# Kernel optimization log

Measured on AMD Instinct MI355X. Metric: run time of the kernel, lower is better.

Reference implementation:

```python
import jax, jax.numpy as jnp
import numpy as np

T, H = 2048, 1024          # tokens, hidden_size
NH, NKV, D = 16, 4, 64     # heads, kv heads, head_dim
E, F = 8, 1024             # experts, intermediate_size
TOPK = 1
EPS = 1e-5
THETA = 500000.0
SCALE = D ** -0.5


def rmsnorm(x, w=None, eps=EPS):
    # fp32 accumulation like vLLM RMSNorm
    v = jnp.mean(x.astype(jnp.float32) ** 2, axis=-1, keepdims=True)
    y = x.astype(jnp.float32) * jax.lax.rsqrt(v + eps)
    y = y.astype(x.dtype)
    return y * w if w is not None else y


def setup_inputs() -> dict:
    key = jax.random.key(0)
    ks = jax.random.split(key, 12)
    s = 1.0 / np.sqrt(H)
    sf = 1.0 / np.sqrt(F)
    return {
        "positions": jnp.arange(T, dtype=jnp.int32),
        "hidden_states": jax.random.normal(ks[0], (T, H), jnp.float32),
        "ln1_w": jnp.ones((H,), jnp.float32),
        "ln2_w": jnp.ones((H,), jnp.float32),
        "wqkv": jax.random.normal(ks[1], (H, (NH + 2 * NKV) * D), jnp.float32) * s,
        "wo": jax.random.normal(ks[2], (NH * D, H), jnp.float32) * s,
        "router_w": jax.random.normal(ks[3], (H, E), jnp.float32) * s,
        "w_gate": jax.random.normal(ks[4], (E, H, F), jnp.float32) * s,
        "w_up": jax.random.normal(ks[5], (E, H, F), jnp.float32) * s,
        "w_down": jax.random.normal(ks[6], (E, F, H), jnp.float32) * sf,
        "sh_gate": jax.random.normal(ks[7], (H, F), jnp.float32) * s,
        "sh_up": jax.random.normal(ks[8], (H, F), jnp.float32) * s,
        "sh_down": jax.random.normal(ks[9], (F, H), jnp.float32) * sf,
    }


def reference(positions, hidden_states, ln1_w, ln2_w, wqkv, wo, router_w,
              w_gate, w_up, w_down, sh_gate, sh_up, sh_down):
    # --- input_layernorm (residual is None on first call) ---
    residual = hidden_states
    h = rmsnorm(hidden_states, ln1_w)

    # --- attention: qkv proj ---
    qkv = h @ wqkv
    q = qkv[:, : NH * D].reshape(T, NH, D)
    k = qkv[:, NH * D: (NH + NKV) * D].reshape(T, NKV, D)
    v = qkv[:, (NH + NKV) * D:].reshape(T, NKV, D)

    # --- neox-style RoPE ---
    half = D // 2
    inv_freq = 1.0 / (THETA ** (jnp.arange(half, dtype=jnp.float32) / half))
    ang = positions.astype(jnp.float32)[:, None] * inv_freq[None, :]
    cos = jnp.cos(ang)[:, None, :]  # [T,1,half]
    sin = jnp.sin(ang)[:, None, :]

    def rope(x):
        x1, x2 = x[..., :half], x[..., half:]
        return jnp.concatenate([x1 * cos - x2 * sin, x2 * cos + x1 * sin], axis=-1)

    q = rope(q)
    k = rope(k)

    # --- fp32 QK-RMSNorm (no weight), applied after RoPE as in source ---
    q = rmsnorm(q)
    k = rmsnorm(k)

    # --- GQA causal attention ---
    n_rep = NH // NKV
    kr = jnp.repeat(k, n_rep, axis=1)  # [T,NH,D]
    vr = jnp.repeat(v, n_rep, axis=1)
    scores = jnp.einsum('thd,shd->hts', q, kr) * SCALE  # [NH,T,T]
    causal = positions[:, None] >= positions[None, :]
    scores = jnp.where(causal[None], scores, -jnp.inf)
    attn = jax.nn.softmax(scores, axis=-1)
    ao = jnp.einsum('hts,shd->thd', attn, vr).reshape(T, NH * D)
    h = ao @ wo

    # --- post_attention_layernorm with fused residual add ---
    x = h + residual
    residual = x
    h = rmsnorm(x, ln2_w)

    # --- MoE: top-1 sigmoid router, router weight applied on input ---
    logits = h @ router_w                      # [T,E]
    score, idx = jax.lax.top_k(logits, TOPK)   # [T,1]
    gate = jax.nn.sigmoid(score.astype(jnp.float32)).astype(h.dtype)
    x_in = h * gate                            # apply_router_weight_on_input
    onehot = (idx == jnp.arange(E)[None, :]).astype(h.dtype)  # [T,E]
    g = jax.nn.silu(jnp.einsum('th,ehf->tef', x_in, w_gate)) \
        * jnp.einsum('th,ehf->tef', x_in, w_up)               # [T,E,F]
    out_e = jnp.einsum('tef,efh->teh', g, w_down)             # [T,E,H]
    routed = jnp.einsum('teh,te->th', out_e, onehot)

    # --- shared expert (SiLU MLP) ---
    shared = (jax.nn.silu(h @ sh_gate) * (h @ sh_up)) @ sh_down

    out = routed + shared
    return (out, residual)
```

## Files before the change

kernel.cpp:

```cpp
#include <hip/hip_runtime.h>
#include <hip/hip_bf16.h>
#include <cmath>
#include <cstdint>

#define T 2048
#define H 1024
#define NH 16
#define NKV 4
#define DH 64
#define NE 8
#define FF 1024
#define QKVN ((NH + 2 * NKV) * DH)
#define EPS 1e-5f
#define ATTN_SCALE 0.125f
#define LOG2E 1.44269504f
#define MBOUND 12.0f

typedef short bf16x8 __attribute__((ext_vector_type(8)));
typedef float floatx4 __attribute__((ext_vector_type(4)));

__device__ __forceinline__ void gload16(const void* g, void* l) {
  __builtin_amdgcn_global_load_lds((const __attribute__((address_space(1))) void*)g,
                                   (__attribute__((address_space(3))) void*)l, 16, 0, 0);
}

__global__ __launch_bounds__(256) void rmsnorm1024(const float* __restrict__ x,
                                                   const float* __restrict__ w,
                                                   __hip_bfloat16* __restrict__ yb) {
  int row = blockIdx.x;
  const float4* x4 = (const float4*)(x + (size_t)row * H);
  float4 v = x4[threadIdx.x];
  float s = v.x * v.x + v.y * v.y + v.z * v.z + v.w * v.w;
  #pragma unroll
  for (int o = 32; o; o >>= 1) s += __shfl_down(s, o, 64);
  __shared__ float red[4];
  if ((threadIdx.x & 63) == 0) red[threadIdx.x >> 6] = s;
  __syncthreads();
  s = red[0] + red[1] + red[2] + red[3];
  float inv = rsqrtf(s * (1.0f / (float)H) + EPS);
  float4 wv = ((const float4*)w)[threadIdx.x];
  __hip_bfloat16* yp = yb + (size_t)row * H + threadIdx.x * 4;
  yp[0] = __float2bfloat16(v.x * inv * wv.x);
  yp[1] = __float2bfloat16(v.y * inv * wv.y);
  yp[2] = __float2bfloat16(v.z * inv * wv.z);
  yp[3] = __float2bfloat16(v.w * inv * wv.w);
}

__global__ __launch_bounds__(256) void fused_add_rms(const float* __restrict__ a,
                                                     const float* __restrict__ b,
                                                     float* __restrict__ resid,
                                                     const float* __restrict__ w,
                                                     float* __restrict__ yf,
                                                     __hip_bfloat16* __restrict__ yb) {
  int row = blockIdx.x;
  float4 av = ((const float4*)(a + (size_t)row * H))[threadIdx.x];
  float4 bv = ((const float4*)(b + (size_t)row * H))[threadIdx.x];
  float4 v = make_float4(av.x + bv.x, av.y + bv.y, av.z + bv.z, av.w + bv.w);
  ((float4*)(resid + (size_t)row * H))[threadIdx.x] = v;
  float s = v.x * v.x + v.y * v.y + v.z * v.z + v.w * v.w;
  #pragma unroll
  for (int o = 32; o; o >>= 1) s += __shfl_down(s, o, 64);
  __shared__ float red[4];
  if ((threadIdx.x & 63) == 0) red[threadIdx.x >> 6] = s;
  __syncthreads();
  s = red[0] + red[1] + red[2] + red[3];
  float inv = rsqrtf(s * (1.0f / (float)H) + EPS);
  float4 wv = ((const float4*)w)[threadIdx.x];
  float o0 = v.x * inv * wv.x, o1 = v.y * inv * wv.y, o2 = v.z * inv * wv.z, o3 = v.w * inv * wv.w;
  ((float4*)(yf + (size_t)row * H))[threadIdx.x] = make_float4(o0, o1, o2, o3);
  __hip_bfloat16* yp = yb + (size_t)row * H + threadIdx.x * 4;
  yp[0] = __float2bfloat16(o0);
  yp[1] = __float2bfloat16(o1);
  yp[2] = __float2bfloat16(o2);
  yp[3] = __float2bfloat16(o3);
}

__global__ __launch_bounds__(256) void tcast9(const float* __restrict__ srcE,
                                              const float* __restrict__ srcS,
                                              __hip_bfloat16* __restrict__ dst, int R, int C,
                                              long long srcStride, long long dstStride,
                                              long long sBatch, long long dBatch) {
  int z = blockIdx.z;
  const float* src = (srcS && z == (int)gridDim.z - 1) ? srcS : srcE + (long long)z * sBatch;
  dst += (long long)z * dBatch;
  int c0 = blockIdx.x * 64, r0 = blockIdx.y * 32;
  __shared__ float tile[32][65];
  int tid = threadIdx.x;
  int lr = tid >> 4;
  int lc = (tid & 15) * 4;
  #pragma unroll
  for (int it = 0; it < 2; it++) {
    float4 v = *(const float4*)(src + (long long)(r0 + lr + it * 16) * srcStride + c0 + lc);
    tile[lr + it * 16][lc + 0] = v.x;
    tile[lr + it * 16][lc + 1] = v.y;
    tile[lr + it * 16][lc + 2] = v.z;
    tile[lr + it * 16][lc + 3] = v.w;
  }
  __syncthreads();
  int oc = tid >> 2;
  int rr = (tid & 3) * 8;
  short ov[8];
  #pragma unroll
  for (int i = 0; i < 8; i++) {
    __hip_bfloat16 b = __float2bfloat16(tile[rr + i][oc]);
    ov[i] = *(short*)&b;
  }
  *(bf16x8*)((short*)dst + (long long)(c0 + oc) * dstStride + r0 + rr) = *(bf16x8*)ov;
}

__global__ __launch_bounds__(256) void gemm_bf16(const __hip_bfloat16* __restrict__ A,
                                                 const __hip_bfloat16* __restrict__ A2,
                                                 const __hip_bfloat16* __restrict__ Bt,
                                                 void* __restrict__ Cout, void* __restrict__ Cout2,
                                                 int M, int N, int K, int out_bf16,
                                                 const int* __restrict__ row_offs,
                                                 long long strideB) {
  int e = blockIdx.z;
  bool sh = (A2 != nullptr && e == (int)gridDim.z - 1);
  int rbeg = 0, rend = M;
  const __hip_bfloat16* Ap = A;
  void* Cp = Cout;
  if (sh) {
    Ap = A2; Cp = Cout2;
  } else if (row_offs) {
    rbeg = row_offs[e]; rend = row_offs[e + 1];
  }
  long long m0 = rbeg + (long long)blockIdx.y * 128;
  if (m0 >= rend) return;
  long long n0 = (long long)blockIdx.x * 64;
  const __hip_bfloat16* Bp = Bt + (long long)e * strideB;

  __shared__ unsigned short As[128 * 64];
  __shared__ unsigned short Bs[64 * 64];

  int tid = threadIdx.x;
  int lane = tid & 63, w = tid >> 6;
  int wr = (w >> 1) * 64, wc = (w & 1) * 32;
  int qd = lane >> 4, ln16 = lane & 15;
  int l7 = ln16 & 7;

  floatx4 acc[4][2];
  floatx4 zero = {0.f, 0.f, 0.f, 0.f};
  #pragma unroll
  for (int i = 0; i < 4; i++)
    #pragma unroll
    for (int j = 0; j < 2; j++) acc[i][j] = zero;

  int rowA[4], kcA[4];
  #pragma unroll
  for (int it = 0; it < 4; it++) {
    int chunk = tid + it * 256;
    rowA[it] = chunk >> 3;
    kcA[it] = ((chunk & 7) ^ (rowA[it] & 7)) * 8;
  }

  for (int k0 = 0; k0 < K; k0 += 64) {
    #pragma unroll
    for (int it = 0; it < 4; it++) {
      long long ra = m0 + rowA[it];
      if (ra >= rend) ra = rend - 1;
      gload16(Ap + ra * K + k0 + kcA[it], As + (tid + it * 256) * 8);
    }
    #pragma unroll
    for (int it = 0; it < 2; it++)
      gload16(Bp + (n0 + rowA[it]) * K + k0 + kcA[it], Bs + (tid + it * 256) * 8);
    __syncthreads();
    #pragma unroll
    for (int s = 0; s < 2; s++) {
      bf16x8 af[4], bfr[2];
      #pragma unroll
      for (int i = 0; i < 4; i++) {
        int row = wr + i * 16 + ln16;
        af[i] = *(const bf16x8*)(As + row * 64 + (((s * 4 + qd) ^ l7) * 8));
      }
      #pragma unroll
      for (int j = 0; j < 2; j++) {
        int row = wc + j * 16 + ln16;
        bfr[j] = *(const bf16x8*)(Bs + row * 64 + (((s * 4 + qd) ^ l7) * 8));
      }
      #pragma unroll
      for (int i = 0; i < 4; i++)
        #pragma unroll
        for (int j = 0; j < 2; j++)
          acc[i][j] = __builtin_amdgcn_mfma_f32_16x16x32_bf16(af[i], bfr[j], acc[i][j], 0, 0, 0);
    }
    __syncthreads();
  }

  #pragma unroll
  for (int i = 0; i < 4; i++) {
    #pragma unroll
    for (int r = 0; r < 4; r++) {
      long long gm = m0 + wr + i * 16 + qd * 4 + r;
      if (gm < rend) {
        #pragma unroll
        for (int j = 0; j < 2; j++) {
          long long gn = n0 + wc + j * 16 + ln16;
          float v = acc[i][j][r];
          if (out_bf16)
            ((__hip_bfloat16*)Cp)[gm * N + gn] = __float2bfloat16(v);
          else
            ((float*)Cp)[gm * N + gn] = v;
        }
      }
    }
  }
}

__global__ __launch_bounds__(256) void rope_pack(const float* __restrict__ qkv,
                                                 const int* __restrict__ positions,
                                                 __hip_bfloat16* __restrict__ Qb,
                                                 __hip_bfloat16* __restrict__ Kb) {
  int b = blockIdx.x * 4 + (threadIdx.x >> 6);
  int t = b / (NH + NKV);
  int hh = b % (NH + NKV);
  const float* ptr = qkv + (long long)t * QKVN + hh * DH;
  int d = threadIdx.x & 63;
  float v = ptr[d];
  int fi = d & 31;
  float inv_freq = exp2f(-(float)fi * (18.93156857f / 32.0f));
  float ang = (float)positions[t] * inv_freq;
  float c = __cosf(ang), s = __sinf(ang);
  float other = __shfl_xor(v, 32, 64);
  float r = (d < 32) ? (v * c - other * s) : (v * c + other * s);
  float sq = r * r;
  #pragma unroll
  for (int off = 32; off; off >>= 1) sq += __shfl_xor(sq, off, 64);
  float o = r * rsqrtf(sq * (1.0f / (float)DH) + EPS);
  if (hh < NH)
    Qb[(size_t)t * (NH * DH) + hh * DH + d] = __float2bfloat16(o * (ATTN_SCALE * LOG2E));
  else
    Kb[(size_t)t * (NKV * DH) + (hh - NH) * DH + d] = __float2bfloat16(o);
}

__global__ __launch_bounds__(256) void attn_mfma(const __hip_bfloat16* __restrict__ Qb,
                                                 const __hip_bfloat16* __restrict__ Kb,
                                                 const __hip_bfloat16* __restrict__ VtG,
                                                 __hip_bfloat16* __restrict__ ao) {
  int h = blockIdx.y;
  int kvh = h >> 2;
  int nb = gridDim.x;
  int bx = blockIdx.x;
  int qi = (bx & 1) ? (nb - 1 - (bx >> 1)) : (bx >> 1);
  int q0 = qi * 64;

  __shared__ unsigned short Ks[64 * 64];
  __shared__ unsigned short Vs[64 * 64];
  __shared__ unsigned short Ps[4 * 16 * 64];

  int tid = threadIdx.x;
  int lane = tid & 63, w = tid >> 6;
  int qd = lane >> 4, ln16 = lane & 15;
  int l7 = ln16 & 7;
  unsigned short* Pw = Ps + w * 16 * 64;

  int r0 = tid >> 3;
  int sc = ((tid & 7) ^ (r0 & 7)) * 8;

  int tq = q0 + w * 16 + ln16;
  const unsigned short* qp = (const unsigned short*)Qb + (size_t)tq * (NH * DH) + h * DH;
  bf16x8 aq[2];
  aq[0] = *(const bf16x8*)(qp + qd * 8);
  aq[1] = *(const bf16x8*)(qp + 32 + qd * 8);

  bf16x8 ones;
  #pragma unroll
  for (int i = 0; i < 8; i++) ones[i] = (short)0x3F80;

  floatx4 O_[4], accl;
  floatx4 zero = {0.f, 0.f, 0.f, 0.f};
  #pragma unroll
  for (int j = 0; j < 4; j++) O_[j] = zero;
  accl = zero;
  int tq_base = q0 + w * 16 + qd * 4;
  int wave_min_row = q0 + w * 16;

  for (int kb = 0; kb < q0 + 64; kb += 64) {
    gload16((const unsigned short*)Kb + (size_t)(kb + r0) * (NKV * DH) + kvh * DH + sc, Ks + tid * 8);
    gload16((const unsigned short*)Kb + (size_t)(kb + r0 + 32) * (NKV * DH) + kvh * DH + sc, Ks + tid * 8 + 2048);
    gload16((const unsigned short*)VtG + (size_t)(kvh * DH + r0) * T + kb + sc, Vs + tid * 8);
    gload16((const unsigned short*)VtG + (size_t)(kvh * DH + r0 + 32) * T + kb + sc, Vs + tid * 8 + 2048);
    __syncthreads();

    floatx4 S_[4];
    #pragma unroll
    for (int j = 0; j < 4; j++) S_[j] = zero;
    #pragma unroll
    for (int s = 0; s < 2; s++) {
      bf16x8 bk[4];
      #pragma unroll
      for (int j = 0; j < 4; j++)
        bk[j] = *(const bf16x8*)(Ks + (j * 16 + ln16) * 64 + (((s * 4 + qd) ^ l7) * 8));
      #pragma unroll
      for (int j = 0; j < 4; j++)
        S_[j] = __builtin_amdgcn_mfma_f32_16x16x32_bf16(aq[s], bk[j], S_[j], 0, 0, 0);
    }

    if (kb + 63 > wave_min_row) {
      #pragma unroll
      for (int j = 0; j < 4; j++) {
        int tk = kb + j * 16 + ln16;
        #pragma unroll
        for (int r = 0; r < 4; r++)
          S_[j][r] = (tk <= tq_base + r) ? exp2f(S_[j][r] - MBOUND) : 0.f;
      }
    } else {
      #pragma unroll
      for (int j = 0; j < 4; j++)
        #pragma unroll
        for (int r = 0; r < 4; r++) S_[j][r] = exp2f(S_[j][r] - MBOUND);
    }

    #pragma unroll
    for (int j = 0; j < 4; j++)
      #pragma unroll
      for (int r = 0; r < 4; r++) {
        int row = qd * 4 + r;
        int pc = (((j * 2 + (ln16 >> 3)) ^ (row & 7)) * 8) + l7;
        __hip_bfloat16 pb = __float2bfloat16(S_[j][r]);
        Pw[row * 64 + pc] = *(unsigned short*)&pb;
      }

    #pragma unroll
    for (int s = 0; s < 2; s++) {
      bf16x8 ap = *(const bf16x8*)(Pw + ln16 * 64 + (((s * 4 + qd) ^ l7) * 8));
      bf16x8 bv[4];
      #pragma unroll
      for (int j = 0; j < 4; j++)
        bv[j] = *(const bf16x8*)(Vs + (j * 16 + ln16) * 64 + (((s * 4 + qd) ^ l7) * 8));
      #pragma unroll
      for (int j = 0; j < 4; j++)
        O_[j] = __builtin_amdgcn_mfma_f32_16x16x32_bf16(ap, bv[j], O_[j], 0, 0, 0);
      accl = __builtin_amdgcn_mfma_f32_16x16x32_bf16(ap, ones, accl, 0, 0, 0);
    }
    __syncthreads();
  }

  float inv[4];
  #pragma unroll
  for (int r = 0; r < 4; r++) inv[r] = 1.0f / accl[r];
  #pragma unroll
  for (int j = 0; j < 4; j++)
    #pragma unroll
    for (int r = 0; r < 4; r++)
      ao[(size_t)(tq_base + r) * (NH * DH) + h * DH + j * 16 + ln16] =
          __float2bfloat16(O_[j][r] * inv[r]);
}

__global__ void silumul_both(const __hip_bfloat16* __restrict__ gA2,
                             const __hip_bfloat16* __restrict__ gS2,
                             __hip_bfloat16* __restrict__ gP,
                             __hip_bfloat16* __restrict__ gPs, int n4each) {
  int i = blockIdx.x * blockDim.x + threadIdx.x;
  const __hip_bfloat16* src = gA2;
  __hip_bfloat16* dst = gP;
  if (i >= n4each) {
    i -= n4each;
    src = gS2;
    dst = gPs;
  }
  int el = i * 4;
  int row = el >> 10;
  int c = el & (FF - 1);
  const __hip_bfloat16* g = src + (size_t)row * (2 * FF) + c;
  #pragma unroll
  for (int k = 0; k < 4; k++) {
    float av = __bfloat162float(g[k]);
    float bv = __bfloat162float(g[FF + k]);
    dst[el + k] = __float2bfloat16(av / (1.f + __expf(-av)) * bv);
  }
}

__global__ __launch_bounds__(64) void router_kernel(const float* __restrict__ h2,
                                                    const float* __restrict__ rw,
                                                    int* __restrict__ idx,
                                                    float* __restrict__ gate,
                                                    int* __restrict__ counts) {
  int t = blockIdx.x;
  int lane = threadIdx.x;
  float acc[NE] = {};
  for (int k = lane; k < H; k += 64) {
    float hv = h2[(long long)t * H + k];
    float4 r0 = *(const float4*)(rw + (long long)k * NE);
    float4 r1 = *(const float4*)(rw + (long long)k * NE + 4);
    acc[0] += hv * r0.x; acc[1] += hv * r0.y; acc[2] += hv * r0.z; acc[3] += hv * r0.w;
    acc[4] += hv * r1.x; acc[5] += hv * r1.y; acc[6] += hv * r1.z; acc[7] += hv * r1.w;
  }
  #pragma unroll
  for (int off = 32; off; off >>= 1)
    #pragma unroll
    for (int e2 = 0; e2 < NE; e2++) acc[e2] += __shfl_down(acc[e2], off, 64);
  if (lane == 0) {
    int best = 0;
    float bv = acc[0];
    #pragma unroll
    for (int e2 = 1; e2 < NE; e2++)
      if (acc[e2] > bv) { bv = acc[e2]; best = e2; }
    idx[t] = best;
    gate[t] = 1.f / (1.f + expf(-bv));
    atomicAdd(&counts[best], 1);
  }
}

__global__ void zero_counts_kernel(int* c) {
  if (threadIdx.x < 2 * NE) c[threadIdx.x] = 0;
}

__global__ void scan_kernel(const int* __restrict__ counts, int* __restrict__ offs) {
  if (threadIdx.x == 0) {
    int s = 0;
    for (int e2 = 0; e2 < NE; e2++) { offs[e2] = s; s += counts[e2]; }
    offs[NE] = s;
  }
}

__global__ void assign_kernel(const int* __restrict__ idx, const int* __restrict__ offs,
                              int* __restrict__ cnt2, int* __restrict__ perm,
                              int* __restrict__ pos) {
  int t = blockIdx.x * blockDim.x + threadIdx.x;
  if (t >= T) return;
  int e2 = idx[t];
  int p = offs[e2] + atomicAdd(&cnt2[e2], 1);
  pos[t] = p;
  perm[p] = t;
}

__global__ __launch_bounds__(256) void gather_kernel(const float* __restrict__ h2,
                                                     const float* __restrict__ gate,
                                                     const int* __restrict__ perm,
                                                     __hip_bfloat16* __restrict__ xg) {
  int p = blockIdx.x;
  int t = perm[p];
  float g = gate[t];
  float4 v = ((const float4*)(h2 + (long long)t * H))[threadIdx.x];
  __hip_bfloat16* yp = xg + (long long)p * H + threadIdx.x * 4;
  yp[0] = __float2bfloat16(v.x * g);
  yp[1] = __float2bfloat16(v.y * g);
  yp[2] = __float2bfloat16(v.z * g);
  yp[3] = __float2bfloat16(v.w * g);
}

__global__ __launch_bounds__(256) void final_add_kernel(float* __restrict__ out,
                                                        const float* __restrict__ outp,
                                                        const int* __restrict__ pos) {
  int t = blockIdx.x;
  int p = pos[t];
  const float4* src = (const float4*)(outp + (long long)p * H);
  float4* dst = (float4*)(out + (long long)t * H);
  float4 a = dst[threadIdx.x];
  float4 b = src[threadIdx.x];
  a.x += b.x; a.y += b.y; a.z += b.z; a.w += b.w;
  dst[threadIdx.x] = a;
}

extern "C" void kernel_launch(void* const* d_in, const int* in_sizes, int n_in,
                              void* d_out, int out_size, void* d_ws, size_t ws_size,
                              hipStream_t stream) {
  const int* positions = (const int*)d_in[0];
  const float* hidden = (const float*)d_in[1];
  const float* ln1_w = (const float*)d_in[2];
  const float* ln2_w = (const float*)d_in[3];
  const float* wqkv = (const float*)d_in[4];
  const float* wo = (const float*)d_in[5];
  const float* router_w = (const float*)d_in[6];
  const float* w_gate = (const float*)d_in[7];
  const float* w_up = (const float*)d_in[8];
  const float* w_down = (const float*)d_in[9];
  const float* sh_gate = (const float*)d_in[10];
  const float* sh_up = (const float*)d_in[11];
  const float* sh_down = (const float*)d_in[12];

  float* out = (float*)d_out;
  float* resid = out + (size_t)T * H;

  char* p = (char*)d_ws;
  auto alloc = [&](size_t bytes) { char* r = p; p += (bytes + 255) & ~(size_t)255; return r; };

  float* qkv = (float*)alloc((size_t)T * QKVN * 4);
  float* h2 = (float*)alloc((size_t)T * H * 4);
  float* gb1 = (float*)alloc((size_t)T * H * 4);
  float* outp = (float*)alloc((size_t)T * H * 4);
  __hip_bfloat16* h1b = (__hip_bfloat16*)alloc((size_t)T * H * 2);
  __hip_bfloat16* aob = (__hip_bfloat16*)alloc((size_t)T * H * 2);
  __hip_bfloat16* h2b = (__hip_bfloat16*)alloc((size_t)T * H * 2);
  __hip_bfloat16* xgb = (__hip_bfloat16*)alloc((size_t)T * H * 2);
  __hip_bfloat16* gA2 = (__hip_bfloat16*)alloc((size_t)T * 2 * FF * 2);
  __hip_bfloat16* gP = (__hip_bfloat16*)alloc((size_t)T * FF * 2);
  __hip_bfloat16* Qb = (__hip_bfloat16*)alloc((size_t)T * NH * DH * 2);
  __hip_bfloat16* Kb = (__hip_bfloat16*)alloc((size_t)T * NKV * DH * 2);
  __hip_bfloat16* VtG = (__hip_bfloat16*)alloc((size_t)NKV * DH * T * 2);
  __hip_bfloat16* wqkvT = (__hip_bfloat16*)alloc((size_t)H * QKVN * 2);
  __hip_bfloat16* woT = (__hip_bfloat16*)alloc((size_t)H * H * 2);
  __hip_bfloat16* wguT = (__hip_bfloat16*)alloc((size_t)9 * 2 * FF * H * 2);
  __hip_bfloat16* wdT = (__hip_bfloat16*)alloc((size_t)9 * H * FF * 2);
  int* counts = (int*)alloc(2 * NE * 4);
  int* cnt2 = counts + NE;
  int* offs = (int*)alloc((NE + 1) * 4);
  int* idx = (int*)alloc(T * 4);
  int* perm = (int*)alloc(T * 4);
  int* pos = (int*)alloc(T * 4);
  float* gate = (float*)alloc(T * 4);

  __hip_bfloat16* gS2 = (__hip_bfloat16*)gb1;
  __hip_bfloat16* gPs = h1b;

  tcast9<<<dim3(QKVN / 64, H / 32, 1), 256, 0, stream>>>(wqkv, nullptr, wqkvT, H, QKVN, QKVN, H, 0, 0);
  tcast9<<<dim3(H / 64, H / 32, 1), 256, 0, stream>>>(wo, nullptr, woT, H, H, H, H, 0, 0);
  tcast9<<<dim3(FF / 64, H / 32, 9), 256, 0, stream>>>(w_gate, sh_gate, wguT, H, FF, FF, H,
                                                       (long long)H * FF, (long long)2 * H * FF);
  tcast9<<<dim3(FF / 64, H / 32, 9), 256, 0, stream>>>(w_up, sh_up, wguT + (size_t)FF * H, H, FF, FF, H,
                                                       (long long)H * FF, (long long)2 * H * FF);
  tcast9<<<dim3(H / 64, FF / 32, 9), 256, 0, stream>>>(w_down, sh_down, wdT, FF, H, H, FF,
                                                       (long long)FF * H, (long long)H * FF);

  rmsnorm1024<<<T, 256, 0, stream>>>(hidden, ln1_w, h1b);
  gemm_bf16<<<dim3(QKVN / 64, T / 128, 1), 256, 0, stream>>>(h1b, nullptr, wqkvT, qkv, nullptr,
                                                             T, QKVN, H, 0, nullptr, 0);
  rope_pack<<<T * (NH + NKV) / 4, 256, 0, stream>>>(qkv, positions, Qb, Kb);
  tcast9<<<dim3(NKV * DH / 64, T / 32, 1), 256, 0, stream>>>(qkv + (NH + NKV) * DH, nullptr, VtG,
                                                             T, NKV * DH, QKVN, T, 0, 0);
  attn_mfma<<<dim3(T / 64, NH), 256, 0, stream>>>(Qb, Kb, VtG, aob);
  gemm_bf16<<<dim3(H / 64, T / 128, 1), 256, 0, stream>>>(aob, nullptr, woT, gb1, nullptr,
                                                          T, H, H, 0, nullptr, 0);
  fused_add_rms<<<T, 256, 0, stream>>>(gb1, hidden, resid, ln2_w, h2, h2b);
  zero_counts_kernel<<<1, 64, 0, stream>>>(counts);
  router_kernel<<<T, 64, 0, stream>>>(h2, router_w, idx, gate, counts);
  scan_kernel<<<1, 64, 0, stream>>>(counts, offs);
  assign_kernel<<<T / 256, 256, 0, stream>>>(idx, offs, cnt2, perm, pos);
  gather_kernel<<<T, 256, 0, stream>>>(h2, gate, perm, xgb);
  gemm_bf16<<<dim3(2 * FF / 64, T / 128, 9), 256, 0, stream>>>(xgb, h2b, wguT, gA2, gS2,
                                                               T, 2 * FF, H, 1, offs,
                                                               (long long)2 * H * FF);
  silumul_both<<<(2 * T * FF / 4) / 256, 256, 0, stream>>>(gA2, gS2, gP, gPs, T * FF / 4);
  gemm_bf16<<<dim3(H / 64, T / 128, 9), 256, 0, stream>>>(gP, gPs, wdT, outp, out,
                                                          T, H, FF, 0, offs, (long long)FF * H);
  final_add_kernel<<<T, 256, 0, stream>>>(out, outp, pos);
}
```

Before: 410.3 us.

## Double-buffer GEMM and attention LDS tiles, scatter MoE down-proj via atomics

Adds two-stage LDS double buffering to the bf16 GEMM and the attention kernel, so the next K/V or A/B tile is prefetched while MFMAs run on the current one. The down-projection GEMM now atomically adds its output straight into the zeroed output at the permuted token row. This removes the separate outp buffer and the final_add kernel. The assign and gather kernels are merged into one launch. The cost is doubled shared memory, which may lower occupancy, plus fp32 atomic traffic and a memset of the output.

```diff
diff --git a/kernel.cpp b/kernel.cpp
--- a/kernel.cpp
+++ b/kernel.cpp
@@ -112,9 +112,10 @@
                                                  const __hip_bfloat16* __restrict__ A2,
                                                  const __hip_bfloat16* __restrict__ Bt,
                                                  void* __restrict__ Cout, void* __restrict__ Cout2,
-                                                 int M, int N, int K, int out_bf16,
+                                                 int M, int N, int K, int out_mode,
                                                  const int* __restrict__ row_offs,
-                                                 long long strideB) {
+                                                 long long strideB,
+                                                 const int* __restrict__ permmap) {
   int e = blockIdx.z;
   bool sh = (A2 != nullptr && e == (int)gridDim.z - 1);
   int rbeg = 0, rend = M;
@@ -130,8 +131,8 @@
   long long n0 = (long long)blockIdx.x * 64;
   const __hip_bfloat16* Bp = Bt + (long long)e * strideB;
 
-  __shared__ unsigned short As[128 * 64];
-  __shared__ unsigned short Bs[64 * 64];
+  __shared__ unsigned short As[2 * 128 * 64];
+  __shared__ unsigned short Bs[2 * 64 * 64];
 
   int tid = threadIdx.x;
   int lane = tid & 63, w = tid >> 6;
@@ -147,36 +148,51 @@
     for (int j = 0; j < 2; j++) acc[i][j] = zero;
 
   int rowA[4], kcA[4];
+  long long raClamp[4];
   #pragma unroll
   for (int it = 0; it < 4; it++) {
     int chunk = tid + it * 256;
     rowA[it] = chunk >> 3;
     kcA[it] = ((chunk & 7) ^ (rowA[it] & 7)) * 8;
-  }
-
-  for (int k0 = 0; k0 < K; k0 += 64) {
-    #pragma unroll
-    for (int it = 0; it < 4; it++) {
-      long long ra = m0 + rowA[it];
-      if (ra >= rend) ra = rend - 1;
-      gload16(Ap + ra * K + k0 + kcA[it], As + (tid + it * 256) * 8);
-    }
-    #pragma unroll
-    for (int it = 0; it < 2; it++)
-      gload16(Bp + (n0 + rowA[it]) * K + k0 + kcA[it], Bs + (tid + it * 256) * 8);
-    __syncthreads();
+    long long ra = m0 + rowA[it];
+    raClamp[it] = (ra >= rend) ? (rend - 1) : ra;
+  }
+
+  int niter = K >> 6;
+  #pragma unroll
+  for (int it = 0; it < 4; it++)
+    gload16(Ap + raClamp[it] * K + kcA[it], As + (tid + it * 256) * 8);
+  #pragma unroll
+  for (int it = 0; it < 2; it++)
+    gload16(Bp + (n0 + rowA[it]) * K + kcA[it], Bs + (tid + it * 256) * 8);
+  __syncthreads();
+
+  for (int k = 0; k < niter; k++) {
+    int cur = k & 1;
+    if (k + 1 < niter) {
+      int nxt = cur ^ 1;
+      int k0 = (k + 1) << 6;
+      #pragma unroll
+      for (int it = 0; it < 4; it++)
+        gload16(Ap + raClamp[it] * K + k0 + kcA[it], As + nxt * 8192 + (tid + it * 256) * 8);
+      #pragma unroll
+      for (int it = 0; it < 2; it++)
+        gload16(Bp + (n0 + rowA[it]) * K + k0 + kcA[it], Bs + nxt * 4096 + (tid + it * 256) * 8);
+    }
+    const unsigned short* Asc = As + cur * 8192;
+    const unsigned short* Bsc = Bs + cur * 4096;
     #pragma unroll
     for (int s = 0; s < 2; s++) {
       bf16x8 af[4], bfr[2];
       #pragma unroll
       for (int i = 0; i < 4; i++) {
         int row = wr + i * 16 + ln16;
-        af[i] = *(const bf16x8*)(As + row * 64 + (((s * 4 + qd) ^ l7) * 8));
+        af[i] = *(const bf16x8*)(Asc + row * 64 + (((s * 4 + qd) ^ l7) * 8));
       }
       #pragma unroll
       for (int j = 0; j < 2; j++) {
         int row = wc + j * 16 + ln16;
-        bfr[j] = *(const bf16x8*)(Bs + row * 64 + (((s * 4 + qd) ^ l7) * 8));
+        bfr[j] = *(const bf16x8*)(Bsc + row * 64 + (((s * 4 + qd) ^ l7) * 8));
       }
       #pragma unroll
       for (int i = 0; i < 4; i++)
@@ -193,12 +209,15 @@
     for (int r = 0; r < 4; r++) {
       long long gm = m0 + wr + i * 16 + qd * 4 + r;
       if (gm < rend) {
+        long long gmo = (out_mode == 2 && !sh && permmap) ? permmap[gm] : gm;
         #pragma unroll
         for (int j = 0; j < 2; j++) {
           long long gn = n0 + wc + j * 16 + ln16;
           float v = acc[i][j][r];
-          if (out_bf16)
+          if (out_mode == 1)
             ((__hip_bfloat16*)Cp)[gm * N + gn] = __float2bfloat16(v);
+          else if (out_mode == 2)
+            atomicAdd(&((float*)Cp)[gmo * N + gn], v);
           else
             ((float*)Cp)[gm * N + gn] = v;
         }
@@ -244,8 +263,8 @@
   int qi = (bx & 1) ? (nb - 1 - (bx >> 1)) : (bx >> 1);
   int q0 = qi * 64;
 
-  __shared__ unsigned short Ks[64 * 64];
-  __shared__ unsigned short Vs[64 * 64];
+  __shared__ unsigned short Ks[2 * 64 * 64];
+  __shared__ unsigned short Vs[2 * 64 * 64];
   __shared__ unsigned short Ps[4 * 16 * 64];
 
   int tid = threadIdx.x;
@@ -275,12 +294,27 @@
   int tq_base = q0 + w * 16 + qd * 4;
   int wave_min_row = q0 + w * 16;
 
+  const unsigned short* KbU = (const unsigned short*)Kb;
+  const unsigned short* VtU = (const unsigned short*)VtG;
+
+  gload16(KbU + (size_t)(r0) * (NKV * DH) + kvh * DH + sc, Ks + tid * 8);
+  gload16(KbU + (size_t)(r0 + 32) * (NKV * DH) + kvh * DH + sc, Ks + tid * 8 + 2048);
+  gload16(VtU + (size_t)(kvh * DH + r0) * T + sc, Vs + tid * 8);
+  gload16(VtU + (size_t)(kvh * DH + r0 + 32) * T + sc, Vs + tid * 8 + 2048);
+  __syncthreads();
+
   for (int kb = 0; kb < q0 + 64; kb += 64) {
-    gload16((const unsigned short*)Kb + (size_t)(kb + r0) * (NKV * DH) + kvh * DH + sc, Ks + tid * 8);
-    gload16((const unsigned short*)Kb + (size_t)(kb + r0 + 32) * (NKV * DH) + kvh * DH + sc, Ks + tid * 8 + 2048);
-    gload16((const unsigned short*)VtG + (size_t)(kvh * DH + r0) * T + kb + sc, Vs + tid * 8);
-    gload16((const unsigned short*)VtG + (size_t)(kvh * DH + r0 + 32) * T + kb + sc, Vs + tid * 8 + 2048);
-    __syncthreads();
+    int cur = (kb >> 6) & 1;
+    if (kb < q0) {
+      int nxt = cur ^ 1;
+      int kn = kb + 64;
+      gload16(KbU + (size_t)(kn + r0) * (NKV * DH) + kvh * DH + sc, Ks + nxt * 4096 + tid * 8);
+      gload16(KbU + (size_t)(kn + r0 + 32) * (NKV * DH) + kvh * DH + sc, Ks + nxt * 4096 + tid * 8 + 2048);
+      gload16(VtU + (size_t)(kvh * DH + r0) * T + kn + sc, Vs + nxt * 4096 + tid * 8);
+      gload16(VtU + (size_t)(kvh * DH + r0 + 32) * T + kn + sc, Vs + nxt * 4096 + tid * 8 + 2048);
+    }
+    const unsigned short* Ksc = Ks + cur * 4096;
+    const unsigned short* Vsc = Vs + cur * 4096;
 
     floatx4 S_[4];
     #pragma unroll
@@ -290,7 +324,7 @@
       bf16x8 bk[4];
       #pragma unroll
       for (int j = 0; j < 4; j++)
-        bk[j] = *(const bf16x8*)(Ks + (j * 16 + ln16) * 64 + (((s * 4 + qd) ^ l7) * 8));
+        bk[j] = *(const bf16x8*)(Ksc + (j * 16 + ln16) * 64 + (((s * 4 + qd) ^ l7) * 8));
       #pragma unroll
       for (int j = 0; j < 4; j++)
         S_[j] = __builtin_amdgcn_mfma_f32_16x16x32_bf16(aq[s], bk[j], S_[j], 0, 0, 0);
@@ -327,7 +361,7 @@
       bf16x8 bv[4];
       #pragma unroll
       for (int j = 0; j < 4; j++)
-        bv[j] = *(const bf16x8*)(Vs + (j * 16 + ln16) * 64 + (((s * 4 + qd) ^ l7) * 8));
+        bv[j] = *(const bf16x8*)(Vsc + (j * 16 + ln16) * 64 + (((s * 4 + qd) ^ l7) * 8));
       #pragma unroll
       for (int j = 0; j < 4; j++)
         O_[j] = __builtin_amdgcn_mfma_f32_16x16x32_bf16(ap, bv[j], O_[j], 0, 0, 0);
@@ -414,23 +448,23 @@
   }
 }
 
-__global__ void assign_kernel(const int* __restrict__ idx, const int* __restrict__ offs,
-                              int* __restrict__ cnt2, int* __restrict__ perm,
-                              int* __restrict__ pos) {
-  int t = blockIdx.x * blockDim.x + threadIdx.x;
-  if (t >= T) return;
-  int e2 = idx[t];
-  int p = offs[e2] + atomicAdd(&cnt2[e2], 1);
-  pos[t] = p;
-  perm[p] = t;
-}
-
-__global__ __launch_bounds__(256) void gather_kernel(const float* __restrict__ h2,
+__global__ __launch_bounds__(256) void assign_gather(const int* __restrict__ idx,
+                                                     const int* __restrict__ offs,
+                                                     int* __restrict__ cnt2,
+                                                     int* __restrict__ perm,
+                                                     const float* __restrict__ h2,
                                                      const float* __restrict__ gate,
-                                                     const int* __restrict__ perm,
                                                      __hip_bfloat16* __restrict__ xg) {
-  int p = blockIdx.x;
-  int t = perm[p];
+  int t = blockIdx.x;
+  __shared__ int ps;
+  if (threadIdx.x == 0) {
+    int e2 = idx[t];
+    int p = offs[e2] + atomicAdd(&cnt2[e2], 1);
+    perm[p] = t;
+    ps = p;
+  }
+  __syncthreads();
+  int p = ps;
   float g = gate[t];
   float4 v = ((const float4*)(h2 + (long long)t * H))[threadIdx.x];
   __hip_bfloat16* yp = xg + (long long)p * H + threadIdx.x * 4;
@@ -438,19 +472,6 @@
   yp[1] = __float2bfloat16(v.y * g);
   yp[2] = __float2bfloat16(v.z * g);
   yp[3] = __float2bfloat16(v.w * g);
-}
-
-__global__ __launch_bounds__(256) void final_add_kernel(float* __restrict__ out,
-                                                        const float* __restrict__ outp,
-                                                        const int* __restrict__ pos) {
-  int t = blockIdx.x;
-  int p = pos[t];
-  const float4* src = (const float4*)(outp + (long long)p * H);
-  float4* dst = (float4*)(out + (long long)t * H);
-  float4 a = dst[threadIdx.x];
-  float4 b = src[threadIdx.x];
-  a.x += b.x; a.y += b.y; a.z += b.z; a.w += b.w;
-  dst[threadIdx.x] = a;
 }
 
 extern "C" void kernel_launch(void* const* d_in, const int* in_sizes, int n_in,
@@ -479,7 +500,6 @@
   float* qkv = (float*)alloc((size_t)T * QKVN * 4);
   float* h2 = (float*)alloc((size_t)T * H * 4);
   float* gb1 = (float*)alloc((size_t)T * H * 4);
-  float* outp = (float*)alloc((size_t)T * H * 4);
   __hip_bfloat16* h1b = (__hip_bfloat16*)alloc((size_t)T * H * 2);
   __hip_bfloat16* aob = (__hip_bfloat16*)alloc((size_t)T * H * 2);
   __hip_bfloat16* h2b = (__hip_bfloat16*)alloc((size_t)T * H * 2);
@@ -498,11 +518,12 @@
   int* offs = (int*)alloc((NE + 1) * 4);
   int* idx = (int*)alloc(T * 4);
   int* perm = (int*)alloc(T * 4);
-  int* pos = (int*)alloc(T * 4);
   float* gate = (float*)alloc(T * 4);
 
   __hip_bfloat16* gS2 = (__hip_bfloat16*)gb1;
   __hip_bfloat16* gPs = h1b;
+
+  hipMemsetAsync(out, 0, (size_t)T * H * sizeof(float), stream);
 
   tcast9<<<dim3(QKVN / 64, H / 32, 1), 256, 0, stream>>>(wqkv, nullptr, wqkvT, H, QKVN, QKVN, H, 0, 0);
   tcast9<<<dim3(H / 64, H / 32, 1), 256, 0, stream>>>(wo, nullptr, woT, H, H, H, H, 0, 0);
@@ -515,24 +536,22 @@
 
   rmsnorm1024<<<T, 256, 0, stream>>>(hidden, ln1_w, h1b);
   gemm_bf16<<<dim3(QKVN / 64, T / 128, 1), 256, 0, stream>>>(h1b, nullptr, wqkvT, qkv, nullptr,
-                                                             T, QKVN, H, 0, nullptr, 0);
+                                                             T, QKVN, H, 0, nullptr, 0, nullptr);
   rope_pack<<<T * (NH + NKV) / 4, 256, 0, stream>>>(qkv, positions, Qb, Kb);
   tcast9<<<dim3(NKV * DH / 64, T / 32, 1), 256, 0, stream>>>(qkv + (NH + NKV) * DH, nullptr, VtG,
                                                              T, NKV * DH, QKVN, T, 0, 0);
   attn_mfma<<<dim3(T / 64, NH), 256, 0, stream>>>(Qb, Kb, VtG, aob);
   gemm_bf16<<<dim3(H / 64, T / 128, 1), 256, 0, stream>>>(aob, nullptr, woT, gb1, nullptr,
-                                                          T, H, H, 0, nullptr, 0);
+                                                          T, H, H, 0, nullptr, 0, nullptr);
   fused_add_rms<<<T, 256, 0, stream>>>(gb1, hidden, resid, ln2_w, h2, h2b);
   zero_counts_kernel<<<1, 64, 0, stream>>>(counts);
   router_kernel<<<T, 64, 0, stream>>>(h2, router_w, idx, gate, counts);
   scan_kernel<<<1, 64, 0, stream>>>(counts, offs);
-  assign_kernel<<<T / 256, 256, 0, stream>>>(idx, offs, cnt2, perm, pos);
-  gather_kernel<<<T, 256, 0, stream>>>(h2, gate, perm, xgb);
+  assign_gather<<<T, 256, 0, stream>>>(idx, offs, cnt2, perm, h2, gate, xgb);
   gemm_bf16<<<dim3(2 * FF / 64, T / 128, 9), 256, 0, stream>>>(xgb, h2b, wguT, gA2, gS2,
                                                                T, 2 * FF, H, 1, offs,
-                                                               (long long)2 * H * FF);
+                                                               (long long)2 * H * FF, nullptr);
   silumul_both<<<(2 * T * FF / 4) / 256, 256, 0, stream>>>(gA2, gS2, gP, gPs, T * FF / 4);
-  gemm_bf16<<<dim3(H / 64, T / 128, 9), 256, 0, stream>>>(gP, gPs, wdT, outp, out,
-                                                          T, H, FF, 0, offs, (long long)FF * H);
-  final_add_kernel<<<T, 256, 0, stream>>>(out, outp, pos);
-}
+  gemm_bf16<<<dim3(H / 64, T / 128, 9), 256, 0, stream>>>(gP, gPs, wdT, out, out,
+                                                          T, H, FF, 2, offs, (long long)FF * H, perm);
+}
```

New measurement: 416.6 us. About the same (+1.5%).
